# Kernel optimization log

Measured on AMD Instinct MI355X. Metric: run time of the kernel, lower is better.

## Reference

```python
import jax, jax.numpy as jnp
import numpy as np

N_NODES = 10000
N_EDGES = 80000
N_GRAPHS = 64
H, D = 4, 512          # num_heads, out_feats
EMB = 768
HFEAT = 512
NCLS = 2
SLOPE = 0.2            # DGL GATConv default negative_slope
BN_EPS = 1e-5


def setup_inputs() -> dict:
    key = jax.random.key(0)
    ks = jax.random.split(key, 24)
    f32 = jnp.float32
    rn = lambda k, s, sc=0.02: jax.random.normal(k, s, dtype=f32) * sc
    inp = {
        "node_feat": jax.random.normal(ks[0], (N_NODES, EMB), dtype=f32),
        "func_feat": jax.random.normal(ks[1], (N_NODES, EMB), dtype=f32),
        "W1": rn(ks[2], (EMB, H * D)),
        "al1": rn(ks[3], (H, D), 0.1),
        "ar1": rn(ks[4], (H, D), 0.1),
        "b1": jnp.zeros((H * D,), f32),
        "W2": rn(ks[5], (H * D, H * D)),
        "al2": rn(ks[6], (H, D), 0.1),
        "ar2": rn(ks[7], (H, D), 0.1),
        "b2": jnp.zeros((H * D,), f32),
        "Wfc": rn(ks[8], (H * D, HFEAT)),
        "bfc": jnp.zeros((HFEAT,), f32),
        "Wfco": rn(ks[9], (EMB, HFEAT)),
        "bfco": jnp.zeros((HFEAT,), f32),
        "Wh": rn(ks[10], (8, HFEAT, HFEAT)),
        "bh": jnp.zeros((8, HFEAT), f32),
        "gamma": jnp.ones((HFEAT,), f32),
        "beta": jnp.zeros((HFEAT,), f32),
        "Whfc": rn(ks[11], (HFEAT, HFEAT)),
        "bhfc": jnp.zeros((HFEAT,), f32),
        "Wf": rn(ks[12], (HFEAT, NCLS)),
        "bf": jnp.zeros((NCLS,), f32),
        "src": jax.random.randint(ks[13], (N_EDGES,), 0, N_NODES),
        "dst": jax.random.randint(ks[14], (N_EDGES,), 0, N_NODES),
        "graph_id": jnp.sort(jax.random.randint(ks[15], (N_NODES,), 0, N_GRAPHS)),
    }
    return inp


def gat_conv(h, W, al, ar, b, src, dst):
    """DGL GATConv (eval mode): fc -> per-head attention logits -> edge
    softmax over incoming edges -> scatter-sum -> +bias. Returns (N, H*D)."""
    feat = (h @ W).reshape(-1, H, D)                      # (N,H,D)
    el = jnp.einsum('nhd,hd->nh', feat, al)               # (N,H)
    er = jnp.einsum('nhd,hd->nh', feat, ar)
    e = jax.nn.leaky_relu(el[src] + er[dst], SLOPE)       # (E,H)
    emax = jax.ops.segment_max(e, dst, num_segments=N_NODES)
    ex = jnp.exp(e - emax[dst])
    den = jax.ops.segment_sum(ex, dst, num_segments=N_NODES)
    a = ex / den[dst]                                     # edge softmax (E,H)
    msg = feat[src] * a[:, :, None]                       # (E,H,D) gather+weight
    out = jax.ops.segment_sum(msg, dst, num_segments=N_NODES)
    return (out + b.reshape(1, H, D)).reshape(-1, H * D)


def reference(node_feat, func_feat, W1, al1, ar1, b1, W2, al2, ar2, b2,
              Wfc, bfc, Wfco, bfco, Wh, bh, gamma, beta, Whfc, bhfc,
              Wf, bf, src, dst, graph_id):
    h = gat_conv(node_feat, W1, al1, ar1, b1, src, dst)   # (N, 2048)
    h = gat_conv(h, W2, al2, ar2, b2, src, dst)           # (N, 2048)
    h = jax.nn.elu(h @ Wfc + bfc)                         # (N, 512)
    h_func = jax.nn.elu(func_feat @ Wfco + bfco)          # (N, 512)
    for i in range(8):
        h = jax.nn.elu(h @ Wh[i] + bh[i])
        h_func = jax.nn.elu(h_func @ Wh[i] + bh[i])       # dead for output (as in torch)
    counts = jax.ops.segment_sum(jnp.ones((N_NODES,), h.dtype), graph_id,
                                 num_segments=N_GRAPHS)
    hg = jax.ops.segment_sum(h, graph_id, num_segments=N_GRAPHS)
    hg = hg / jnp.maximum(counts, 1.0)[:, None]           # dgl.mean_nodes (G, 512)
    # BatchNorm1d eval with running_mean=0, running_var=1
    hg = hg / jnp.sqrt(1.0 + BN_EPS) * gamma + beta
    hg = jax.nn.elu(hg @ Whfc + bhfc)
    return hg @ Wf + bf                                   # (G, NCLS)
```

## Files before the change

### kernel.cpp

```cpp
#include <hip/hip_runtime.h>
#include <hip/hip_bf16.h>
#include <math.h>

#define N_NODES 10000
#define N_EDGES 80000
#define N_GRAPHS 64
#define NH 4
#define HD 512
#define HDTOT 2048
#define EMB 768
#define HFEAT 512
#define MAXDEG 512

typedef _Float16 half8 __attribute__((ext_vector_type(8)));
typedef _Float16 half4 __attribute__((ext_vector_type(4)));
typedef float f32x4 __attribute__((ext_vector_type(4)));

__device__ __forceinline__ void gload_lds16(const void* g, void* l) {
  __builtin_amdgcn_global_load_lds(
      (const __attribute__((address_space(1))) unsigned int*)g,
      (__attribute__((address_space(3))) unsigned int*)l, 16, 0, 0);
}

__device__ __forceinline__ void wgbar() {
  asm volatile("" ::: "memory");
  __builtin_amdgcn_s_barrier();
  asm volatile("" ::: "memory");
}

template <int N>
__device__ __forceinline__ void vmwait() {
  asm volatile("s_waitcnt vmcnt(%0)" ::"n"(N) : "memory");
}

template <int BM>
__global__ __launch_bounds__(256) void gemm_f16_kernel(
    const _Float16* __restrict__ A, const _Float16* __restrict__ BT,
    const float* __restrict__ bias, _Float16* __restrict__ C,
    int M, int N, int K, int act) {
  constexpr int WR = (BM == 128) ? 2 : 1;
  constexpr int WC = 4 / WR;
  constexpr int MI = (BM / WR) / 16;
  constexpr int NI = (128 / WC) / 16;
  constexpr int NW = NI * 16;
  constexpr int CS = NW + 4;
  constexpr int GPR = NW / 8;

  __shared__ _Float16 smem[(BM + 128) * 64];
  _Float16* As = smem;
  _Float16* Bs = smem + BM * 64;

  const int bn = blockIdx.x * 128, bm = blockIdx.y * BM;
  const int t = threadIdx.x;
  const int lane = t & 63, wave = t >> 6;
  const int wr = wave / WC, wc = wave % WC;
  const int m0 = wr * (BM / WR), n0 = wc * NW;
  const int fr = lane & 15, fq = lane >> 4;

  f32x4 acc[MI][NI];
#pragma unroll
  for (int i = 0; i < MI; ++i)
#pragma unroll
    for (int j = 0; j < NI; ++j) acc[i][j] = (f32x4){0.f, 0.f, 0.f, 0.f};

  for (int k0 = 0; k0 < K; k0 += 64) {
    __syncthreads();
#pragma unroll
    for (int it = 0; it < BM / 32; ++it) {
      int gid = it * 256 + t;
      int r = gid >> 3;
      int q = (gid & 7) ^ (r & 7);
      int grow = bm + r;
      if (grow >= M) grow = M - 1;
      gload_lds16(A + (size_t)grow * K + k0 + q * 8,
                  &As[(it * 256 + wave * 64) * 8]);
    }
#pragma unroll
    for (int it = 0; it < 4; ++it) {
      int gid = it * 256 + t;
      int r = gid >> 3;
      int q = (gid & 7) ^ (r & 7);
      gload_lds16(BT + (size_t)(bn + r) * K + k0 + q * 8,
                  &Bs[(it * 256 + wave * 64) * 8]);
    }
    __syncthreads();

#pragma unroll
    for (int kk = 0; kk < 2; ++kk) {
      half8 af[MI], bf[NI];
#pragma unroll
      for (int mi = 0; mi < MI; ++mi) {
        int m = m0 + mi * 16 + fr;
        af[mi] = *(const half8*)&As[m * 64 + (((kk * 4 + fq) ^ (m & 7))) * 8];
      }
#pragma unroll
      for (int ni = 0; ni < NI; ++ni) {
        int n = n0 + ni * 16 + fr;
        bf[ni] = *(const half8*)&Bs[n * 64 + (((kk * 4 + fq) ^ (n & 7))) * 8];
      }
#pragma unroll
      for (int mi = 0; mi < MI; ++mi)
#pragma unroll
        for (int ni = 0; ni < NI; ++ni)
          acc[mi][ni] = __builtin_amdgcn_mfma_f32_16x16x32_f16(
              af[mi], bf[ni], acc[mi][ni], 0, 0, 0);
    }
  }
  __syncthreads();
  _Float16* cs = smem + wave * 16 * CS;
#pragma unroll
  for (int mi = 0; mi < MI; ++mi) {
#pragma unroll
    for (int ni = 0; ni < NI; ++ni) {
      float bb = bias ? bias[bn + n0 + ni * 16 + fr] : 0.f;
#pragma unroll
      for (int j = 0; j < 4; ++j) {
        float v = acc[mi][ni][j] + bb;
        if (act == 1) v = v > 0.f ? v : expm1f(v);
        cs[(fq * 4 + j) * CS + ni * 16 + fr] = (_Float16)v;
      }
    }
#pragma unroll
    for (int i = 0; i < NW / 32; ++i) {
      int piece = i * 64 + lane;
      int r = piece / GPR, g = piece % GPR;
      int grow = bm + m0 + mi * 16 + r;
      if (grow < M) {
        half8 v = *(const half8*)&cs[r * CS + g * 8];
        *(half8*)&C[(size_t)grow * N + bn + n0 + g * 8] = v;
      }
    }
  }
}

#define GP_SLOT 8192

__global__ __launch_bounds__(512, 1) void gemm256p_f16_kernel(
    const _Float16* __restrict__ A, const _Float16* __restrict__ BT,
    const float* __restrict__ bias, _Float16* __restrict__ C,
    int M, int N, int K, int act, int nbx) {
  __shared__ _Float16 smem[8 * GP_SLOT];

  int flat = blockIdx.x;
  int nwg = gridDim.x;
  if ((nwg & 7) == 0) flat = (flat & 7) * (nwg >> 3) + (flat >> 3);
  const int bn = (flat % nbx) * 256;
  const int bm = (flat / nbx) * 256;

  const int t = threadIdx.x;
  const int lane = t & 63, wave = t >> 6;
  const int wr = wave >> 2, wc = wave & 3;
  const int m0 = wr * 128, n0 = wc * 64;
  const int fr = lane & 15, fq = lane >> 4;

  const _Float16* sA[2];
  const _Float16* sB[2];
#pragma unroll
  for (int it = 0; it < 2; ++it) {
    int gi = it * 512 + t;
    int r = gi >> 2;
    int g = (gi & 3) ^ ((r >> 1) & 3);
    int ra = bm + r;
    if (ra >= M) ra = M - 1;
    sA[it] = A + (size_t)ra * K + g * 8;
    sB[it] = BT + (size_t)(bn + r) * K + g * 8;
  }
  const int ldsbase = (wave * 64) * 8;

  int offA[8], offB[4];
#pragma unroll
  for (int mi = 0; mi < 8; ++mi) {
    int m = m0 + mi * 16 + fr;
    offA[mi] = m * 32 + ((fq ^ ((m >> 1) & 3)) << 3);
  }
#pragma unroll
  for (int ni = 0; ni < 4; ++ni) {
    int n = n0 + ni * 16 + fr;
    offB[ni] = n * 32 + ((fq ^ ((n >> 1) & 3)) << 3);
  }

  f32x4 acc[8][4];
#pragma unroll
  for (int i = 0; i < 8; ++i)
#pragma unroll
    for (int j = 0; j < 4; ++j) acc[i][j] = (f32x4){0.f, 0.f, 0.f, 0.f};

#define STAGE_HALF(kt, wh)                                                  \
  do {                                                                      \
    _Float16* dst_ = smem + ((((kt)&1) * 4 + (wh)) * GP_SLOT);              \
    const _Float16* s0_ = ((wh)&1) ? sB[0] : sA[0];                         \
    const _Float16* s1_ = ((wh)&1) ? sB[1] : sA[1];                         \
    size_t ko_ = (size_t)(kt)*64 + (((wh) >> 1) * 32);                      \
    gload_lds16(s0_ + ko_, &dst_[ldsbase]);                                 \
    gload_lds16(s1_ + ko_, &dst_[4096 + ldsbase]);                          \
  } while (0)

#define PHASE_MFMA(Ah, Bh, MB)                                              \
  do {                                                                      \
    half8 af_[4], bf_[4];                                                   \
    _Pragma("unroll") for (int i_ = 0; i_ < 4; ++i_)                        \
        af_[i_] = *(const half8*)&(Ah)[offA[(MB) + i_]];                    \
    _Pragma("unroll") for (int n_ = 0; n_ < 4; ++n_)                        \
        bf_[n_] = *(const half8*)&(Bh)[offB[n_]];                           \
    __builtin_amdgcn_s_setprio(1);                                          \
    _Pragma("unroll") for (int i_ = 0; i_ < 4; ++i_)                        \
        _Pragma("unroll") for (int n_ = 0; n_ < 4; ++n_)                    \
            acc[(MB) + i_][n_] = __builtin_amdgcn_mfma_f32_16x16x32_f16(    \
                af_[i_], bf_[n_], acc[(MB) + i_][n_], 0, 0, 0);             \
    __builtin_amdgcn_s_setprio(0);                                          \
  } while (0)

  const int NT = K >> 6;

  STAGE_HALF(0, 0);
  STAGE_HALF(0, 1);
  STAGE_HALF(0, 2);
  STAGE_HALF(0, 3);
  vmwait<4>();
  wgbar();

  for (int tt = 0; tt < NT; ++tt) {
    const bool more = (tt + 1 < NT);
    const _Float16* base = smem + (tt & 1) * 4 * GP_SLOT;
    const _Float16* A0 = base;
    const _Float16* B0 = base + GP_SLOT;
    const _Float16* A1 = base + 2 * GP_SLOT;
    const _Float16* B1 = base + 3 * GP_SLOT;

    if (more) STAGE_HALF(tt + 1, 0);
    PHASE_MFMA(A0, B0, 0);
    wgbar();
    if (more) STAGE_HALF(tt + 1, 1);
    PHASE_MFMA(A0, B0, 4);
    if (more) vmwait<4>();
    else vmwait<0>();
    wgbar();
    if (more) STAGE_HALF(tt + 1, 2);
    PHASE_MFMA(A1, B1, 0);
    wgbar();
    if (more) STAGE_HALF(tt + 1, 3);
    PHASE_MFMA(A1, B1, 4);
    if (more) vmwait<4>();
    wgbar();
  }
#undef STAGE_HALF
#undef PHASE_MFMA

  constexpr int CS = 68;
  _Float16* cs = smem + wave * 16 * CS;
#pragma unroll
  for (int mi = 0; mi < 8; ++mi) {
#pragma unroll
    for (int ni = 0; ni < 4; ++ni) {
      float bb = bias ? bias[bn + n0 + ni * 16 + fr] : 0.f;
#pragma unroll
      for (int j = 0; j < 4; ++j) {
        float v = acc[mi][ni][j] + bb;
        if (act == 1) v = v > 0.f ? v : expm1f(v);
        cs[(fq * 4 + j) * CS + ni * 16 + fr] = (_Float16)v;
      }
    }
#pragma unroll
    for (int i = 0; i < 2; ++i) {
      int piece = i * 64 + lane;
      int r = piece >> 3, g = piece & 7;
      int grow = bm + m0 + mi * 16 + r;
      if (grow < M) {
        half8 v = *(const half8*)&cs[r * CS + g * 8];
        *(half8*)&C[(size_t)grow * N + bn + n0 + g * 8] = v;
      }
    }
  }
}

__global__ __launch_bounds__(256) void convert_wt_kernel(
    const float* __restrict__ W, _Float16* __restrict__ WT, int K, int N) {
  __shared__ float tile[32][33];
  W += (size_t)blockIdx.z * K * N;
  WT += (size_t)blockIdx.z * K * N;
  int k0 = blockIdx.x * 32, n0 = blockIdx.y * 32;
  int t = threadIdx.x;
  int r = t >> 3, c4 = (t & 7) * 4;
  float4 v = *(const float4*)(W + (size_t)(k0 + r) * N + n0 + c4);
  tile[r][c4 + 0] = v.x;
  tile[r][c4 + 1] = v.y;
  tile[r][c4 + 2] = v.z;
  tile[r][c4 + 3] = v.w;
  __syncthreads();
  float x0 = tile[c4 + 0][r], x1 = tile[c4 + 1][r];
  float x2 = tile[c4 + 2][r], x3 = tile[c4 + 3][r];
  size_t o = (size_t)(n0 + r) * K + k0 + c4;
  *(half4*)&WT[o] = (half4){(_Float16)x0, (_Float16)x1, (_Float16)x2, (_Float16)x3};
}

__global__ void convert_f32_f16_kernel(const float* __restrict__ x,
                                       _Float16* __restrict__ y, int n4) {
  int gid = blockIdx.x * blockDim.x + threadIdx.x;
  if (gid >= n4) return;
  float4 v = *(const float4*)(x + gid * 4);
  *(half4*)(y + gid * 4) =
      (half4){(_Float16)v.x, (_Float16)v.y, (_Float16)v.z, (_Float16)v.w};
}

__global__ void hist_kernel(const int* __restrict__ dst, int* __restrict__ cnt, int E) {
  int gid = blockIdx.x * blockDim.x + threadIdx.x;
  if (gid < E) atomicAdd(&cnt[dst[gid]], 1);
}

__global__ void scan_kernel(const int* __restrict__ cnt, int* __restrict__ row_ptr,
                            int* __restrict__ cursor, int n) {
  __shared__ int part[256];
  int t = threadIdx.x;
  int chunk = (n + 255) / 256;
  int s0 = t * chunk;
  int s1 = min(s0 + chunk, n);
  int sum = 0;
  for (int i = s0; i < s1; ++i) sum += cnt[i];
  part[t] = sum;
  __syncthreads();
  if (t == 0) {
    int acc = 0;
    for (int i = 0; i < 256; ++i) { int v = part[i]; part[i] = acc; acc += v; }
    row_ptr[n] = acc;
  }
  __syncthreads();
  int run = part[t];
  for (int i = s0; i < s1; ++i) {
    row_ptr[i] = run;
    cursor[i] = run;
    run += cnt[i];
  }
}

__global__ void scatter_kernel(const int* __restrict__ src, const int* __restrict__ dst,
                               int* __restrict__ cursor, int* __restrict__ csr_src,
                               int E) {
  int gid = blockIdx.x * blockDim.x + threadIdx.x;
  if (gid < E) {
    int d = dst[gid];
    int pos = atomicAdd(&cursor[d], 1);
    csr_src[pos] = src[gid];
  }
}

__global__ __launch_bounds__(256) void el_er_kernel(
    const _Float16* __restrict__ feat, const float* __restrict__ al,
    const float* __restrict__ ar, float* __restrict__ el, float* __restrict__ er) {
  int n = blockIdx.x;
  int t = threadIdx.x;
  int h = t >> 6, lane = t & 63;
  half8 f = *(const half8*)(feat + (size_t)n * HDTOT + h * HD + lane * 8);
  const float* ap = al + h * HD + lane * 8;
  const float* rp = ar + h * HD + lane * 8;
  float4 a0 = *(const float4*)ap, a1 = *(const float4*)(ap + 4);
  float4 r0 = *(const float4*)rp, r1 = *(const float4*)(rp + 4);
  float f0 = (float)f[0], f1 = (float)f[1], f2 = (float)f[2], f3 = (float)f[3];
  float f4 = (float)f[4], f5 = (float)f[5], f6 = (float)f[6], f7 = (float)f[7];
  float sl = f0 * a0.x + f1 * a0.y + f2 * a0.z + f3 * a0.w +
             f4 * a1.x + f5 * a1.y + f6 * a1.z + f7 * a1.w;
  float sr = f0 * r0.x + f1 * r0.y + f2 * r0.z + f3 * r0.w +
             f4 * r1.x + f5 * r1.y + f6 * r1.z + f7 * r1.w;
  for (int off = 32; off; off >>= 1) {
    sl += __shfl_down(sl, off);
    sr += __shfl_down(sr, off);
  }
  if (lane == 0) {
    el[n * NH + h] = sl;
    er[n * NH + h] = sr;
  }
}

__global__ __launch_bounds__(256) void softmax_aggregate_kernel(
    const _Float16* __restrict__ feat, const float* __restrict__ el,
    const float* __restrict__ er, const int* __restrict__ row_ptr,
    const int* __restrict__ csr_src, float* __restrict__ e_buf,
    const float* __restrict__ bias, _Float16* __restrict__ out) {
  __shared__ float wl[NH][MAXDEG];
  int n = blockIdx.x;
  int t = threadIdx.x;
  int h = t >> 6, lane = t & 63;
  int s = row_ptr[n], epos = row_ptr[n + 1];
  int deg = epos - s;
  bool lds_w = (deg <= MAXDEG);

  if (deg > 0) {
    float ern = er[n * NH + h];
    if (deg <= 64) {
      int p = s + lane;
      bool on = lane < deg;
      float logit = 0.f;
      float m = -INFINITY;
      if (on) {
        float v = el[csr_src[p] * NH + h] + ern;
        logit = v >= 0.f ? v : 0.2f * v;
        m = logit;
      }
#pragma unroll
      for (int off = 32; off; off >>= 1) m = fmaxf(m, __shfl_xor(m, off));
      float ex = on ? expf(logit - m) : 0.f;
      float sum = ex;
#pragma unroll
      for (int off = 32; off; off >>= 1) sum += __shfl_xor(sum, off);
      float inv = 1.f / sum;
      if (on) wl[h][lane] = ex * inv;
    } else if (lds_w) {
      float m = -INFINITY;
      for (int p = s + lane; p < epos; p += 64) {
        float v = el[csr_src[p] * NH + h] + ern;
        v = v >= 0.f ? v : 0.2f * v;
        wl[h][p - s] = v;
        m = fmaxf(m, v);
      }
      for (int off = 32; off; off >>= 1) m = fmaxf(m, __shfl_xor(m, off));
      float sum = 0.f;
      for (int p = s + lane; p < epos; p += 64) {
        float ex = expf(wl[h][p - s] - m);
        wl[h][p - s] = ex;
        sum += ex;
      }
      for (int off = 32; off; off >>= 1) sum += __shfl_xor(sum, off);
      float inv = 1.f / sum;
      for (int p = s + lane; p < epos; p += 64) wl[h][p - s] *= inv;
    } else {
      float m = -INFINITY;
      for (int p = s + lane; p < epos; p += 64) {
        float v = el[csr_src[p] * NH + h] + ern;
        v = v >= 0.f ? v : 0.2f * v;
        e_buf[p * NH + h] = v;
        m = fmaxf(m, v);
      }
      for (int off = 32; off; off >>= 1) m = fmaxf(m, __shfl_xor(m, off));
      float sum = 0.f;
      for (int p = s + lane; p < epos; p += 64) {
        float ex = expf(e_buf[p * NH + h] - m);
        e_buf[p * NH + h] = ex;
        sum += ex;
      }
      for (int off = 32; off; off >>= 1) sum += __shfl_xor(sum, off);
      float inv = 1.f / sum;
      for (int p = s + lane; p < epos; p += 64) e_buf[p * NH + h] *= inv;
    }
  }
  __syncthreads();

  int base = t * 8;
  float acc[8] = {0.f, 0.f, 0.f, 0.f, 0.f, 0.f, 0.f, 0.f};
  int p = s;
  for (; p + 4 <= epos; p += 4) {
    int q = p - s;
    int sn0 = csr_src[p + 0], sn1 = csr_src[p + 1];
    int sn2 = csr_src[p + 2], sn3 = csr_src[p + 3];
    float a0 = lds_w ? wl[h][q + 0] : e_buf[(p + 0) * NH + h];
    float a1 = lds_w ? wl[h][q + 1] : e_buf[(p + 1) * NH + h];
    float a2 = lds_w ? wl[h][q + 2] : e_buf[(p + 2) * NH + h];
    float a3 = lds_w ? wl[h][q + 3] : e_buf[(p + 3) * NH + h];
    half8 f0 = *(const half8*)(feat + (size_t)sn0 * HDTOT + base);
    half8 f1 = *(const half8*)(feat + (size_t)sn1 * HDTOT + base);
    half8 f2 = *(const half8*)(feat + (size_t)sn2 * HDTOT + base);
    half8 f3 = *(const half8*)(feat + (size_t)sn3 * HDTOT + base);
#pragma unroll
    for (int i = 0; i < 8; ++i)
      acc[i] += a0 * (float)f0[i] + a1 * (float)f1[i] +
                a2 * (float)f2[i] + a3 * (float)f3[i];
  }
  for (; p < epos; ++p) {
    int sn = csr_src[p];
    float a = lds_w ? wl[h][p - s] : e_buf[p * NH + h];
    half8 f = *(const half8*)(feat + (size_t)sn * HDTOT + base);
#pragma unroll
    for (int i = 0; i < 8; ++i) acc[i] += a * (float)f[i];
  }
  float4 b0 = *(const float4*)(bias + base);
  float4 b1 = *(const float4*)(bias + base + 4);
  half8 o;
  o[0] = (_Float16)(acc[0] + b0.x); o[1] = (_Float16)(acc[1] + b0.y);
  o[2] = (_Float16)(acc[2] + b0.z); o[3] = (_Float16)(acc[3] + b0.w);
  o[4] = (_Float16)(acc[4] + b1.x); o[5] = (_Float16)(acc[5] + b1.y);
  o[6] = (_Float16)(acc[6] + b1.z); o[7] = (_Float16)(acc[7] + b1.w);
  *(half8*)(out + (size_t)n * HDTOT + base) = o;
}

__global__ __launch_bounds__(512) void pool_final_kernel(
    const _Float16* __restrict__ hfeat, const int* __restrict__ graph_id,
    const float* __restrict__ gamma, const float* __restrict__ beta,
    const float* __restrict__ Whfc, const float* __restrict__ bhfc,
    const float* __restrict__ Wf, const float* __restrict__ bf,
    float* __restrict__ out) {
  __shared__ float sh[HFEAT];
  __shared__ float st[HFEAT];
  __shared__ float r0[8], r1[8];
  __shared__ int s_lo, s_hi;
  int g = blockIdx.x, t = threadIdx.x;
  if (t == 0) {
    int lo = 0, hi = N_NODES;
    while (lo < hi) { int m = (lo + hi) >> 1; if (graph_id[m] < g) lo = m + 1; else hi = m; }
    s_lo = lo;
    int lo2 = lo, hi2 = N_NODES;
    while (lo2 < hi2) { int m = (lo2 + hi2) >> 1; if (graph_id[m] < g + 1) lo2 = m + 1; else hi2 = m; }
    s_hi = lo2;
  }
  __syncthreads();
  int lo = s_lo, hi = s_hi;
  int col = t;
  float acc = 0.f;
  for (int n = lo; n < hi; ++n) acc += (float)hfeat[(size_t)n * HFEAT + col];
  float invc = 1.f / fmaxf((float)(hi - lo), 1.f);
  float bnscale = rsqrtf(1.f + 1e-5f);
  sh[col] = acc * invc * bnscale * gamma[col] + beta[col];
  __syncthreads();
  float a2 = bhfc[col];
  for (int k = 0; k < HFEAT; ++k) a2 += sh[k] * Whfc[k * HFEAT + col];
  st[col] = a2 > 0.f ? a2 : expm1f(a2);
  __syncthreads();
  float p0 = st[col] * Wf[col * 2 + 0];
  float p1 = st[col] * Wf[col * 2 + 1];
  for (int off = 32; off; off >>= 1) {
    p0 += __shfl_down(p0, off);
    p1 += __shfl_down(p1, off);
  }
  int w = t >> 6;
  if ((t & 63) == 0) { r0[w] = p0; r1[w] = p1; }
  __syncthreads();
  if (t == 0) {
    float q0 = bf[0], q1 = bf[1];
#pragma unroll
    for (int i = 0; i < 8; ++i) { q0 += r0[i]; q1 += r1[i]; }
    out[g * 2 + 0] = q0;
    out[g * 2 + 1] = q1;
  }
}

static void gemm_raw(const _Float16* A, const _Float16* wt, const float* bias,
                     _Float16* C, int M, int N, int K, int act,
                     bool small_m_tile, hipStream_t stream) {
  if (small_m_tile) {
    dim3 grid(N / 128, (M + 63) / 64);
    hipLaunchKernelGGL(gemm_f16_kernel<64>, grid, dim3(256), 0, stream,
                       A, wt, bias, C, M, N, K, act);
  } else {
    dim3 grid(N / 128, (M + 127) / 128);
    hipLaunchKernelGGL(gemm_f16_kernel<128>, grid, dim3(256), 0, stream,
                       A, wt, bias, C, M, N, K, act);
  }
}

static void gemm(const _Float16* A, const float* W, _Float16* wt,
                 const float* bias, _Float16* C, int M, int N, int K, int act,
                 bool small_m_tile, hipStream_t stream) {
  hipLaunchKernelGGL(convert_wt_kernel, dim3(K / 32, N / 32, 1), dim3(256),
                     0, stream, W, wt, K, N);
  gemm_raw(A, wt, bias, C, M, N, K, act, small_m_tile, stream);
}

static void gemm_big(const _Float16* A, const float* W, _Float16* wt,
                     const float* bias, _Float16* C, int M, int N, int K,
                     int act, hipStream_t stream) {
  hipLaunchKernelGGL(convert_wt_kernel, dim3(K / 32, N / 32, 1), dim3(256),
                     0, stream, W, wt, K, N);
  if (N == 2048 && M > 8192 && (K & 63) == 0) {
    int nbx = N / 256;
    hipLaunchKernelGGL(gemm256p_f16_kernel, dim3(256), dim3(512), 0, stream,
                       A, wt, bias, C, 8192, N, K, act, nbx);
    int rem = M - 8192;
    dim3 grid(N / 128, (rem + 127) / 128);
    hipLaunchKernelGGL(gemm_f16_kernel<128>, grid, dim3(256), 0, stream,
                       A + (size_t)8192 * K, wt, bias,
                       C + (size_t)8192 * N, rem, N, K, act);
  } else {
    gemm_raw(A, wt, bias, C, M, N, K, act, false, stream);
  }
}

static void gat_layer(const _Float16* h_in, int K_in, const float* W, _Float16* wt,
                      const float* al, const float* ar, const float* b,
                      const int* row_ptr, const int* csr_src,
                      _Float16* featbuf, float* el, float* er,
                      float* e_buf, _Float16* out, hipStream_t stream) {
  gemm_big(h_in, W, wt, nullptr, featbuf, N_NODES, HDTOT, K_in, 0, stream);
  hipLaunchKernelGGL(el_er_kernel, dim3(N_NODES), dim3(256), 0, stream, featbuf, al, ar, el, er);
  hipLaunchKernelGGL(softmax_aggregate_kernel, dim3(N_NODES), dim3(256), 0, stream,
                     featbuf, el, er, row_ptr, csr_src, e_buf, b, out);
}

extern "C" void kernel_launch(void* const* d_in, const int* in_sizes, int n_in,
                              void* d_out, int out_size, void* d_ws, size_t ws_size,
                              hipStream_t stream) {
  const float* node_feat = (const float*)d_in[0];
  const float* W1 = (const float*)d_in[2];
  const float* al1 = (const float*)d_in[3];
  const float* ar1 = (const float*)d_in[4];
  const float* b1 = (const float*)d_in[5];
  const float* W2 = (const float*)d_in[6];
  const float* al2 = (const float*)d_in[7];
  const float* ar2 = (const float*)d_in[8];
  const float* b2 = (const float*)d_in[9];
  const float* Wfc = (const float*)d_in[10];
  const float* bfc = (const float*)d_in[11];
  const float* Wh = (const float*)d_in[14];
  const float* bh = (const float*)d_in[15];
  const float* gamma = (const float*)d_in[16];
  const float* beta = (const float*)d_in[17];
  const float* Whfc = (const float*)d_in[18];
  const float* bhfc = (const float*)d_in[19];
  const float* Wf = (const float*)d_in[20];
  const float* bf = (const float*)d_in[21];
  const int* src = (const int*)d_in[22];
  const int* dst = (const int*)d_in[23];
  const int* graph_id = (const int*)d_in[24];
  float* out = (float*)d_out;

  _Float16* P0 = (_Float16*)d_ws;
  _Float16* P1 = P0 + (size_t)N_NODES * HDTOT;
  _Float16* Pin = P1 + (size_t)N_NODES * HDTOT;
  _Float16* wt = Pin + (size_t)N_NODES * EMB;
  _Float16* whh = wt + (size_t)2048 * 2048;
  float* el = (float*)(whh + (size_t)8 * HFEAT * HFEAT);
  float* er = el + N_NODES * NH;
  float* e_buf = er + N_NODES * NH;
  int* cnt = (int*)(e_buf + (size_t)N_EDGES * NH);
  int* row_ptr = cnt + N_NODES;
  int* cursor = row_ptr + N_NODES + 1;
  int* csr_src = cursor + N_NODES;

  hipMemsetAsync(cnt, 0, N_NODES * sizeof(int), stream);
  hipLaunchKernelGGL(hist_kernel, dim3((N_EDGES + 255) / 256), dim3(256), 0, stream,
                     dst, cnt, N_EDGES);
  hipLaunchKernelGGL(scan_kernel, dim3(1), dim3(256), 0, stream, cnt, row_ptr, cursor, N_NODES);
  hipLaunchKernelGGL(scatter_kernel, dim3((N_EDGES + 255) / 256), dim3(256), 0, stream,
                     src, dst, cursor, csr_src, N_EDGES);

  int n4 = N_NODES * EMB / 4;
  hipLaunchKernelGGL(convert_f32_f16_kernel, dim3((n4 + 255) / 256), dim3(256), 0, stream,
                     node_feat, Pin, n4);
  hipLaunchKernelGGL(convert_wt_kernel, dim3(HFEAT / 32, HFEAT / 32, 8),
                     dim3(256), 0, stream, Wh, whh, HFEAT, HFEAT);

  gat_layer(Pin, EMB, W1, wt, al1, ar1, b1, row_ptr, csr_src,
            P0, el, er, e_buf, P1, stream);
  gat_layer(P1, HDTOT, W2, wt, al2, ar2, b2, row_ptr, csr_src,
            P0, el, er, e_buf, P1, stream);

  gemm(P1, Wfc, wt, bfc, P0, N_NODES, HFEAT, HDTOT, 1, true, stream);

  _Float16* cur = P0;
  _Float16* nxt = P1;
  for (int i = 0; i < 8; ++i) {
    gemm_raw(cur, whh + (size_t)i * HFEAT * HFEAT, bh + (size_t)i * HFEAT, nxt,
             N_NODES, HFEAT, HFEAT, 1, true, stream);
    _Float16* tmp = cur; cur = nxt; nxt = tmp;
  }

  hipLaunchKernelGGL(pool_final_kernel, dim3(N_GRAPHS), dim3(512), 0, stream,
                     cur, graph_id, gamma, beta, Whfc, bhfc, Wf, bf, out);
}
```

Measured before the change: 738.0 us.

## Restructure GEMM main loop phases with explicit barriers and LDS waits

```diff
diff --git a/kernel.cpp b/kernel.cpp
--- a/kernel.cpp
+++ b/kernel.cpp
@@ -195,19 +195,25 @@
     gload_lds16(s1_ + ko_, &dst_[4096 + ldsbase]);                          \
   } while (0)
 
-#define PHASE_MFMA(Ah, Bh, MB)                                              \
+#define PHASE(APTR, BPTR, MB, STAGE_STMT, VM_STMT)                          \
   do {                                                                      \
     half8 af_[4], bf_[4];                                                   \
     _Pragma("unroll") for (int i_ = 0; i_ < 4; ++i_)                        \
-        af_[i_] = *(const half8*)&(Ah)[offA[(MB) + i_]];                    \
+        af_[i_] = *(const half8*)&(APTR)[offA[(MB) + i_]];                  \
     _Pragma("unroll") for (int n_ = 0; n_ < 4; ++n_)                        \
-        bf_[n_] = *(const half8*)&(Bh)[offB[n_]];                           \
+        bf_[n_] = *(const half8*)&(BPTR)[offB[n_]];                         \
+    STAGE_STMT;                                                             \
+    wgbar();                                                                \
+    asm volatile("s_waitcnt lgkmcnt(0)" ::: "memory");                      \
+    __builtin_amdgcn_sched_barrier(0);                                      \
     __builtin_amdgcn_s_setprio(1);                                          \
     _Pragma("unroll") for (int i_ = 0; i_ < 4; ++i_)                        \
         _Pragma("unroll") for (int n_ = 0; n_ < 4; ++n_)                    \
             acc[(MB) + i_][n_] = __builtin_amdgcn_mfma_f32_16x16x32_f16(    \
                 af_[i_], bf_[n_], acc[(MB) + i_][n_], 0, 0, 0);             \
     __builtin_amdgcn_s_setprio(0);                                          \
+    VM_STMT;                                                                \
+    wgbar();                                                                \
   } while (0)
 
   const int NT = K >> 6;
@@ -227,24 +233,15 @@
     const _Float16* A1 = base + 2 * GP_SLOT;
     const _Float16* B1 = base + 3 * GP_SLOT;
 
-    if (more) STAGE_HALF(tt + 1, 0);
-    PHASE_MFMA(A0, B0, 0);
-    wgbar();
-    if (more) STAGE_HALF(tt + 1, 1);
-    PHASE_MFMA(A0, B0, 4);
-    if (more) vmwait<4>();
-    else vmwait<0>();
-    wgbar();
-    if (more) STAGE_HALF(tt + 1, 2);
-    PHASE_MFMA(A1, B1, 0);
-    wgbar();
-    if (more) STAGE_HALF(tt + 1, 3);
-    PHASE_MFMA(A1, B1, 4);
-    if (more) vmwait<4>();
-    wgbar();
+    PHASE(A0, B0, 0, if (more) STAGE_HALF(tt + 1, 0), (void)0);
+    PHASE(A0, B0, 4, if (more) STAGE_HALF(tt + 1, 1),
+          if (more) vmwait<4>(); else vmwait<0>());
+    PHASE(A1, B1, 0, if (more) STAGE_HALF(tt + 1, 2), (void)0);
+    PHASE(A1, B1, 4, if (more) STAGE_HALF(tt + 1, 3),
+          if (more) vmwait<4>());
   }
 #undef STAGE_HALF
-#undef PHASE_MFMA
+#undef PHASE
 
   constexpr int CS = 68;
   _Float16* cs = smem + wave * 16 * CS;
@@ -640,13 +637,13 @@
   gat_layer(P1, HDTOT, W2, wt, al2, ar2, b2, row_ptr, csr_src,
             P0, el, er, e_buf, P1, stream);
 
-  gemm(P1, Wfc, wt, bfc, P0, N_NODES, HFEAT, HDTOT, 1, true, stream);
+  gemm(P1, Wfc, wt, bfc, P0, N_NODES, HFEAT, HDTOT, 1, false, stream);
 
   _Float16* cur = P0;
   _Float16* nxt = P1;
   for (int i = 0; i < 8; ++i) {
     gemm_raw(cur, whh + (size_t)i * HFEAT * HFEAT, bh + (size_t)i * HFEAT, nxt,
-             N_NODES, HFEAT, HFEAT, 1, true, stream);
+             N_NODES, HFEAT, HFEAT, 1, false, stream);
     _Float16* tmp = cur; cur = nxt; nxt = tmp;
   }
 
```

Measured after the change: 784.9 us. 1.06x slower.
